# Kernel tuning notes

Measured on AMD Instinct MI355X. Metric: run time of the kernel, lower is better.

The kernel has to match this reference:

```python
import jax, jax.numpy as jnp
import numpy as np

B, T, D = 2, 512, 512
NUM_SCALES, MIN_S, MAX_S = 10, 0.01, 1.0
SCALES_NP = np.logspace(np.log10(MIN_S), np.log10(MAX_S), NUM_SCALES)


def _golay():
    # extended Golay (24,12) generator exactly as in _initialize_golay_code
    G = np.zeros((12, 24), np.float32)
    for i in range(12):
        G[i, i] = 1.0
        for j in range(11):
            G[i, 12 + j] = (i + j) % 2
        G[i, 23] = G[i, :23].sum() % 2
    return jnp.asarray(G)

GOLAY = _golay()  # [12,24]


def setup_inputs() -> dict:
    key = jax.random.key(0)
    ks = jax.random.split(key, 6)
    return {
        'token_ids': jax.random.randint(ks[0], (B, T), 0, 1000000, dtype=jnp.int32),
        'resonances': jax.random.uniform(ks[1], (D,), minval=1.0, maxval=50.0, dtype=jnp.float32),
        'emb_scales': jnp.ones((D,), jnp.float32),
        'emb_shifts': jnp.zeros((D,), jnp.float32),
        'emb_norm': jnp.ones((1,), jnp.float32),
        'scale_weights': jnp.ones((NUM_SCALES,), jnp.float32),
        'fractal_bias': jnp.zeros((1,), jnp.float32),
        'frac_norm': jnp.ones((1,), jnp.float32),
        'W_enc': jax.random.normal(ks[2], (D, 24), jnp.float32) / np.float32(np.sqrt(D)),
        'b_enc': jnp.zeros((24,), jnp.float32),
        'W_dec': jax.random.normal(ks[3], (24, D), jnp.float32) / np.float32(np.sqrt(24)),
        'b_dec': jnp.zeros((D,), jnp.float32),
        'ecc_strength': jnp.full((1,), 0.1, jnp.float32),
        'energy_preservation': jnp.ones((1,), jnp.float32),
    }


def _fractal_dimension(signal, scale_weights, fractal_bias, frac_norm):
    # differentiable box-counting (GenuineFractalAnalyzer.compute_fractal_dimension)
    input_energy = jnp.linalg.norm(signal)
    s = signal.reshape(-1)  # [N]
    s = (s - s.min()) / (s.max() - s.min() + 1e-8)
    counts = []
    for scale_np in SCALES_NP:
        nb = int(round(1.0 / scale_np))  # static per scale: 100 ... 1
        edges = jnp.linspace(0.0, 1.0, nb + 1)
        lo, hi = edges[:-1][:, None], edges[1:][:, None]  # [nb,1]
        # vectorized over boxes instead of python loop over boxes
        in_box = jax.nn.sigmoid(10.0 * (s[None, :] - lo)) * jax.nn.sigmoid(10.0 * (hi - s[None, :]))  # [nb,N]
        occ = in_box.sum(axis=1)  # [nb]
        counts.append(jax.nn.sigmoid(occ - 0.5).sum())
    box_counts = jnp.stack(counts)  # [NUM_SCALES]
    weighted = box_counts * jax.nn.softmax(scale_weights)
    scales = jnp.asarray(SCALES_NP, jnp.float32)
    log_x = jnp.log(1.0 / scales)
    log_y = jnp.log(weighted + 1e-8)
    n = np.float32(NUM_SCALES)
    sx, sy = log_x.sum(), log_y.sum()
    sxy, sx2 = (log_x * log_y).sum(), (log_x ** 2).sum()
    slope = (n * sxy - sx * sy) / (n * sx2 - sx ** 2 + 1e-8)
    fd = jnp.clip(-slope + fractal_bias, 1.0, 2.5)  # [1]
    out_energy = jnp.linalg.norm(fd)
    return fd * frac_norm * input_energy / out_energy


def reference(token_ids, resonances, emb_scales, emb_shifts, emb_norm, scale_weights,
              fractal_bias, frac_norm, W_enc, b_enc, W_dec, b_dec, ecc_strength,
              energy_preservation):
    # --- GenuineEmbedding.batch_encode (vectorized over B,T,D) ---
    token_value = (token_ids % 1000000).astype(jnp.float32) / 1e6  # [B,T]
    pos = jnp.arange(T, dtype=jnp.float32)  # [T]
    angle = resonances[None, None, :] * (token_value[:, :, None] + pos[None, :, None])  # [B,T,D]
    c, sn = jnp.cos(angle), jnp.sin(angle)
    comp = c * (1.0 + sn) + sn * sn
    emb = comp * emb_scales + emb_shifts
    tok_norm = jnp.linalg.norm(emb, axis=-1, keepdims=True)
    emb = jnp.where(tok_norm > 0, emb * emb_norm / tok_norm, emb)

    # --- GenuineLeechLattice.encode_to_lattice ---
    ecc = ecc_strength[0]
    ep = energy_preservation[0]
    e_in = jnp.linalg.norm(emb, axis=-1, keepdims=True)  # b t 1
    proj = emb @ W_enc + b_enc  # [B,T,24]
    golay_enc = jnp.einsum('btl,kl->btk', proj, GOLAY)  # [B,T,12]
    latt = jnp.round(golay_enc / ecc) * ecc
    e_out = jnp.linalg.norm(latt, axis=-1, keepdims=True)
    latt = latt * (e_in / (e_out + 1e-8)) * ep

    # --- GenuineLeechLattice.decode_from_lattice ---
    e_in2 = jnp.linalg.norm(latt, axis=-1, keepdims=True)
    golay_dec = jnp.einsum('btk,kl->btl', latt, GOLAY)  # [B,T,24]
    corrected = jnp.where(jnp.abs(golay_dec) > ecc, golay_dec, 0.0)
    res = corrected @ W_dec + b_dec  # [B,T,D]
    e_out2 = jnp.linalg.norm(res, axis=-1, keepdims=True)
    res = res * (e_in2 / (e_out2 + 1e-8)) * ep

    # --- GenuineFractalAnalyzer on the corrected signal, then modulate ---
    fd = _fractal_dimension(res, scale_weights, fractal_bias, frac_norm)  # [1]
    return res * fd
```

## Files before the change

kernel.cpp:

```cpp
#include <hip/hip_runtime.h>
#include <math.h>

#define NT   1024
#define TT   512
#define DD   512


__device__ __forceinline__ float np_pairwise512(const float* x, int tid) {
    float r = 0.0f;
    if (tid < 32) {
        const int b = tid >> 3, j = tid & 7;
        const float* p = x + 128 * b + j;
        r = p[0];
        #pragma unroll
        for (int i = 1; i < 16; i++) r = __fadd_rn(r, p[8 * i]);
    }
    r = __fadd_rn(r, __shfl_down(r, 1, 64));
    r = __fadd_rn(r, __shfl_down(r, 2, 64));
    r = __fadd_rn(r, __shfl_down(r, 4, 64));
    r = __fadd_rn(r, __shfl_down(r, 8, 64));
    r = __fadd_rn(r, __shfl_down(r, 16, 64));
    return r;
}

__device__ __forceinline__ float np_pairwise12(const float* a) {
    float r = __fadd_rn(__fadd_rn(__fadd_rn(a[0], a[1]), __fadd_rn(a[2], a[3])),
                        __fadd_rn(__fadd_rn(a[4], a[5]), __fadd_rn(a[6], a[7])));
    r = __fadd_rn(r, a[8]);
    r = __fadd_rn(r, a[9]);
    r = __fadd_rn(r, a[10]);
    r = __fadd_rn(r, a[11]);
    return r;
}

__global__ __launch_bounds__(512, 8) void token_kernel(
    const int*   __restrict__ token_ids,
    const float* __restrict__ resonances,
    const float* __restrict__ emb_scales,
    const float* __restrict__ emb_shifts,
    const float* __restrict__ emb_norm,
    const float* __restrict__ W_enc,
    const float* __restrict__ b_enc,
    const float* __restrict__ W_dec,
    const float* __restrict__ b_dec,
    const float* __restrict__ ecc_p,
    const float* __restrict__ ep_p,
    float*       __restrict__ out,
    double*      __restrict__ partials)
{
    const int tok  = blockIdx.x;
    const int t    = tok % TT;
    const int tid  = threadIdx.x;
    const int lane = tid & 63;
    const int wave = tid >> 6;

    __shared__ float  sh_e[DD];
    __shared__ float  sh_x[DD];
    __shared__ float  sh_p[24];
    __shared__ float  sh_c[24];
    __shared__ float  sh_l[12];
    __shared__ float  sh_sc[4];
    __shared__ double sh_red[8];

    const float ecc   = ecc_p[0];
    const float ep    = ep_p[0];
    const float enorm = emb_norm[0];

    const int   idv  = token_ids[tok];
    const float tv   = __fdiv_rn((float)idv, 1000000.0f);
    const float base = __fadd_rn(tv, (float)t);

    float e0;
    {
        const float a0 = __fmul_rn(resonances[tid], base);
        double s0d, c0d;
        sincos((double)a0, &s0d, &c0d);
        const float s0 = (float)s0d, c0 = (float)c0d;
        const float comp0 = __fadd_rn(__fmul_rn(c0, __fadd_rn(1.0f, s0)), __fmul_rn(s0, s0));
        e0 = __fadd_rn(__fmul_rn(comp0, emb_scales[tid]), emb_shifts[tid]);
    }
    sh_x[tid] = __fmul_rn(e0, e0);
    __syncthreads();

    float ps = np_pairwise512(sh_x, tid);
    if (tid == 0) sh_sc[0] = __fsqrt_rn(ps);
    __syncthreads();
    const float tok_norm = sh_sc[0];
    if (tok_norm > 0.0f)
        e0 = __fdiv_rn(__fmul_rn(e0, enorm), tok_norm);
    sh_e[tid] = e0;
    sh_x[tid] = __fmul_rn(e0, e0);
    __syncthreads();

    ps = np_pairwise512(sh_x, tid);
    const float e_in = __fsqrt_rn(ps);
    __syncthreads();

    if (tid < 24) {
        float acc = 0.0f;
        #pragma unroll 8
        for (int d = 0; d < DD; d++)
            acc = fmaf(sh_e[d], W_enc[d * 24 + tid], acc);
        sh_p[tid] = __fadd_rn(acc, b_enc[tid]);
    }
    __syncthreads();

    if (tid < 12) {
        const int k = tid;
        float g = sh_p[k];
        #pragma unroll
        for (int l = 12; l < 23; l++)
            if ((k + l) & 1) g = __fadd_rn(g, sh_p[l]);
        if (k & 1) g = __fadd_rn(g, sh_p[23]);
        sh_l[k] = __fmul_rn(rintf(__fdiv_rn(g, ecc)), ecc);
    }
    __syncthreads();

    if (tid == 0) {
        float sq[12];
        #pragma unroll
        for (int k = 0; k < 12; k++) sq[k] = __fmul_rn(sh_l[k], sh_l[k]);
        const float e_out = __fsqrt_rn(np_pairwise12(sq));
        const float m1 = __fdiv_rn(e_in, __fadd_rn(e_out, 1e-8f));
        #pragma unroll
        for (int k = 0; k < 12; k++) {
            const float lv = __fmul_rn(__fmul_rn(sh_l[k], m1), ep);
            sh_l[k] = lv;
            sq[k] = __fmul_rn(lv, lv);
        }
        sh_sc[2] = __fsqrt_rn(np_pairwise12(sq));
    }
    __syncthreads();

    if (tid < 24) {
        const int l = tid;
        float g;
        if (l < 12) {
            g = sh_l[l];
        } else if (l < 23) {
            g = 0.0f;
            #pragma unroll
            for (int k = 0; k < 12; k++)
                if ((k + l) & 1) g = __fadd_rn(g, sh_l[k]);
        } else {
            g = 0.0f;
            for (int k = 1; k < 12; k += 2) g = __fadd_rn(g, sh_l[k]);
        }
        sh_c[l] = (fabsf(g) > ecc) ? g : 0.0f;
    }
    __syncthreads();

    float r0 = 0.0f;
    #pragma unroll
    for (int l = 0; l < 24; l++)
        r0 = fmaf(sh_c[l], W_dec[l * DD + tid], r0);
    r0 = __fadd_rn(r0, b_dec[tid]);
    sh_x[tid] = __fmul_rn(r0, r0);
    __syncthreads();
    ps = np_pairwise512(sh_x, tid);
    if (tid == 0) sh_sc[3] = __fsqrt_rn(ps);
    __syncthreads();

    const float m2 = __fdiv_rn(sh_sc[2], __fadd_rn(sh_sc[3], 1e-8f));
    const float f0 = __fmul_rn(__fmul_rn(r0, m2), ep);
    out[tok * DD + tid] = f0;

    double v4 = (double)f0 * (double)f0;
    for (int off = 32; off > 0; off >>= 1) v4 += __shfl_down(v4, off, 64);
    if (lane == 0) sh_red[wave] = v4;
    __syncthreads();
    if (tid == 0) {
        double s = sh_red[0];
        #pragma unroll
        for (int w = 1; w < 8; w++) s += sh_red[w];
        partials[tok] = s;
    }
}

__global__ __launch_bounds__(256) void scale_kernel(
    float*        __restrict__ out,
    const double* __restrict__ partials,
    const float*  __restrict__ frac_norm)
{
    const int tid = threadIdx.x;
    __shared__ double sh[4];
    __shared__ float sh_factor;
    double s = 0.0;
    #pragma unroll
    for (int i = 0; i < 4; i++) s += partials[tid + 256 * i];
    for (int off = 32; off > 0; off >>= 1) s += __shfl_down(s, off, 64);
    if ((tid & 63) == 0) sh[tid >> 6] = s;
    __syncthreads();
    if (tid == 0)
        sh_factor = (float)((double)frac_norm[0] * sqrt(sh[0] + sh[1] + sh[2] + sh[3]));
    __syncthreads();
    const float factor = sh_factor;

    const int i = blockIdx.x * blockDim.x + tid;
    float4 r = ((const float4*)out)[i];
    r.x = __fmul_rn(r.x, factor);
    r.y = __fmul_rn(r.y, factor);
    r.z = __fmul_rn(r.z, factor);
    r.w = __fmul_rn(r.w, factor);
    ((float4*)out)[i] = r;
}

extern "C" void kernel_launch(void* const* d_in, const int* in_sizes, int n_in,
                              void* d_out, int out_size, void* d_ws, size_t ws_size,
                              hipStream_t stream)
{
    const int*   token_ids  = (const int*)  d_in[0];
    const float* resonances = (const float*)d_in[1];
    const float* emb_scales = (const float*)d_in[2];
    const float* emb_shifts = (const float*)d_in[3];
    const float* emb_norm   = (const float*)d_in[4];
    const float* frac_norm  = (const float*)d_in[7];
    const float* W_enc      = (const float*)d_in[8];
    const float* b_enc      = (const float*)d_in[9];
    const float* W_dec      = (const float*)d_in[10];
    const float* b_dec      = (const float*)d_in[11];
    const float* ecc        = (const float*)d_in[12];
    const float* ep         = (const float*)d_in[13];

    double* partials = (double*)d_ws;

    token_kernel<<<NT, 512, 0, stream>>>(token_ids, resonances, emb_scales, emb_shifts,
                                         emb_norm, W_enc, b_enc, W_dec, b_dec, ecc, ep,
                                         (float*)d_out, partials);
    scale_kernel<<<(NT * DD) / 1024, 256, 0, stream>>>((float*)d_out, partials, frac_norm);
}
```

Baseline: 105.3 us.

## Stage W_enc in shared memory and fuse lattice stages into one wave

Each block now copies the full 512x24 encoder weight matrix into shared memory with float4 loads. The 24 serial encoder dot products then read from LDS rather than doing strided global loads. The Golay encode, rounding, energy rescale and Golay decode steps are merged into wave 0 using cross-lane shuffles, which removes several block-wide barriers and the small shared scratch arrays. In exchange, each block uses about 50 KB of LDS, which lowers blocks per CU, and every block redundantly pulls 48 KB from L2.

```diff
diff --git a/kernel.cpp b/kernel.cpp
--- a/kernel.cpp
+++ b/kernel.cpp
@@ -33,7 +33,7 @@
     return r;
 }
 
-__global__ __launch_bounds__(512, 8) void token_kernel(
+__global__ __launch_bounds__(512, 6) void token_kernel(
     const int*   __restrict__ token_ids,
     const float* __restrict__ resonances,
     const float* __restrict__ emb_scales,
@@ -54,13 +54,20 @@
     const int lane = tid & 63;
     const int wave = tid >> 6;
 
+    __shared__ float  sh_w[DD * 24];
     __shared__ float  sh_e[DD];
     __shared__ float  sh_x[DD];
-    __shared__ float  sh_p[24];
     __shared__ float  sh_c[24];
-    __shared__ float  sh_l[12];
     __shared__ float  sh_sc[4];
     __shared__ double sh_red[8];
+
+    {
+        const float4* src = (const float4*)W_enc;
+        float4*       dst = (float4*)sh_w;
+        #pragma unroll
+        for (int i = 0; i < 6; i++)
+            dst[tid + 512 * i] = src[tid + 512 * i];
+    }
 
     const float ecc   = ecc_p[0];
     const float ep    = ep_p[0];
@@ -94,59 +101,69 @@
 
     ps = np_pairwise512(sh_x, tid);
     const float e_in = __fsqrt_rn(ps);
-    __syncthreads();
-
-    if (tid < 24) {
-        float acc = 0.0f;
-        #pragma unroll 8
-        for (int d = 0; d < DD; d++)
-            acc = fmaf(sh_e[d], W_enc[d * 24 + tid], acc);
-        sh_p[tid] = __fadd_rn(acc, b_enc[tid]);
-    }
-    __syncthreads();
-
-    if (tid < 12) {
-        const int k = tid;
-        float g = sh_p[k];
-        #pragma unroll
-        for (int l = 12; l < 23; l++)
-            if ((k + l) & 1) g = __fadd_rn(g, sh_p[l]);
-        if (k & 1) g = __fadd_rn(g, sh_p[23]);
-        sh_l[k] = __fmul_rn(rintf(__fdiv_rn(g, ecc)), ecc);
-    }
-    __syncthreads();
-
-    if (tid == 0) {
-        float sq[12];
-        #pragma unroll
-        for (int k = 0; k < 12; k++) sq[k] = __fmul_rn(sh_l[k], sh_l[k]);
-        const float e_out = __fsqrt_rn(np_pairwise12(sq));
-        const float m1 = __fdiv_rn(e_in, __fadd_rn(e_out, 1e-8f));
-        #pragma unroll
-        for (int k = 0; k < 12; k++) {
-            const float lv = __fmul_rn(__fmul_rn(sh_l[k], m1), ep);
-            sh_l[k] = lv;
-            sq[k] = __fmul_rn(lv, lv);
-        }
-        sh_sc[2] = __fsqrt_rn(np_pairwise12(sq));
-    }
-    __syncthreads();
-
-    if (tid < 24) {
-        const int l = tid;
-        float g;
-        if (l < 12) {
-            g = sh_l[l];
-        } else if (l < 23) {
-            g = 0.0f;
+
+    if (wave == 0) {
+        float p = 0.0f;
+        if (lane < 24) {
+            float acc = 0.0f;
+            #pragma unroll 8
+            for (int d = 0; d < DD; d++)
+                acc = fmaf(sh_e[d], sh_w[d * 24 + lane], acc);
+            p = __fadd_rn(acc, b_enc[lane]);
+        }
+
+        float latt = 0.0f;
+        {
+            const int k = lane;
+            float g = p;
             #pragma unroll
-            for (int k = 0; k < 12; k++)
-                if ((k + l) & 1) g = __fadd_rn(g, sh_l[k]);
-        } else {
-            g = 0.0f;
-            for (int k = 1; k < 12; k += 2) g = __fadd_rn(g, sh_l[k]);
-        }
-        sh_c[l] = (fabsf(g) > ecc) ? g : 0.0f;
+            for (int l = 12; l < 23; l++) {
+                const float v = __shfl(p, l, 64);
+                if ((k + l) & 1) g = __fadd_rn(g, v);
+            }
+            const float v23 = __shfl(p, 23, 64);
+            if (k & 1) g = __fadd_rn(g, v23);
+            latt = __fmul_rn(rintf(__fdiv_rn(g, ecc)), ecc);
+        }
+
+        float lt[12];
+        #pragma unroll
+        for (int k = 0; k < 12; k++) lt[k] = __shfl(latt, k, 64);
+        float m1;
+        {
+            float sq[12];
+            #pragma unroll
+            for (int k = 0; k < 12; k++) sq[k] = __fmul_rn(lt[k], lt[k]);
+            const float e_out = __fsqrt_rn(np_pairwise12(sq));
+            m1 = __fdiv_rn(e_in, __fadd_rn(e_out, 1e-8f));
+        }
+        m1 = __shfl(m1, 0, 64);
+        float lv[12];
+        #pragma unroll
+        for (int k = 0; k < 12; k++) lv[k] = __fmul_rn(__fmul_rn(lt[k], m1), ep);
+        if (lane == 0) {
+            float sq[12];
+            #pragma unroll
+            for (int k = 0; k < 12; k++) sq[k] = __fmul_rn(lv[k], lv[k]);
+            sh_sc[2] = __fsqrt_rn(np_pairwise12(sq));
+        }
+
+        if (lane < 24) {
+            const int l = lane;
+            float g;
+            if (l < 12) {
+                g = lv[l];
+            } else if (l < 23) {
+                g = 0.0f;
+                #pragma unroll
+                for (int k = 0; k < 12; k++)
+                    if ((k + l) & 1) g = __fadd_rn(g, lv[k]);
+            } else {
+                g = 0.0f;
+                for (int k = 1; k < 12; k += 2) g = __fadd_rn(g, lv[k]);
+            }
+            sh_c[l] = (fabsf(g) > ecc) ? g : 0.0f;
+        }
     }
     __syncthreads();
 
```

Measured after the change: 102.9 us. -2.3%, faster.
